# Kernel optimization log

Measured on AMD Instinct MI355X. Metric: run time of the kernel, lower is better.

Reference implementation:

```python
import jax, jax.numpy as jnp
import numpy as np

N = 20000      # nodes
E = 320000     # edges
IN = 128       # in_channels
HID = 64       # hidden_channels (per-head out dim, concat=False -> mean over heads)
HEADS = 4
NEG_SLOPE = 0.2


def setup_inputs() -> dict:
    key = jax.random.key(0)
    ks = jax.random.split(key, 18)
    g = lambda i, shape: jax.random.normal(ks[i], shape, dtype=jnp.float32) * 0.05
    return {
        "x": jax.random.normal(ks[0], (N, IN), dtype=jnp.float32),
        "edge_index": jax.random.randint(ks[1], (2, E), 0, N),
        # GATConv params: lin weight (no bias in PyG lin), att_src/att_dst, out bias
        "W0": g(2, (IN, HEADS * HID)),
        "W1": g(3, (HID, HEADS * HID)),
        "W2": g(4, (HID, HEADS * HID)),
        "W3": g(5, (HID, HEADS * HID)),
        "a_src": g(6, (4, HEADS, HID)),
        "a_dst": g(7, (4, HEADS, HID)),
        "gat_b": g(8, (4, HID)),
        # residual projection for layer 0 (in_channels != hidden_channels)
        "res_W": g(9, (IN, HID)),
        "res_b": g(10, (HID,)),
        # edge classifier MLP: 2*HID -> HID -> HID -> 1
        "lin_W0": g(11, (2 * HID, HID)),
        "lin_b0": g(12, (HID,)),
        "lin_W1": g(13, (HID, HID)),
        "lin_b1": g(14, (HID,)),
        "lin_W2": g(15, (HID, 1)),
        "lin_b2": g(16, (1,)),
    }


def gat_conv(x, src, dst, W, asrc, adst, b, n):
    # x: [n, F_in]; src/dst: [E_tot] (self-loops included); W: [F_in, H*C]
    h = (x @ W).reshape(n, HEADS, HID)                     # [n, H, C]
    s_src = (h * asrc).sum(-1)                             # [n, H]
    s_dst = (h * adst).sum(-1)                             # [n, H]
    e = jax.nn.leaky_relu(s_src[src] + s_dst[dst], NEG_SLOPE)  # [E_tot, H]
    # segment softmax over incoming edges of each dst node
    m = jax.ops.segment_max(e, dst, num_segments=n)        # [n, H]
    p = jnp.exp(e - m[dst])
    z = jax.ops.segment_sum(p, dst, num_segments=n)
    alpha = p / z[dst]                                     # [E_tot, H]
    out = jax.ops.segment_sum(alpha[:, :, None] * h[src], dst, num_segments=n)  # [n, H, C]
    return out.mean(axis=1) + b                            # concat=False -> mean over heads


def reference(x, edge_index, W0, W1, W2, W3, a_src, a_dst, gat_b,
              res_W, res_b, lin_W0, lin_b0, lin_W1, lin_b1, lin_W2, lin_b2):
    n = x.shape[0]
    loop = jnp.arange(n)
    src = jnp.concatenate([edge_index[0], loop])  # PyG GATConv adds self-loops
    dst = jnp.concatenate([edge_index[1], loop])
    Ws = [W0, W1, W2, W3]
    h = x
    for i in range(4):
        h_prev = h
        h = gat_conv(h, src, dst, Ws[i], a_src[i], a_dst[i], gat_b[i], n)
        if i == 0:
            h = h + h_prev @ res_W + res_b   # projected residual
        else:
            h = h + h_prev
        h = jax.nn.elu(h)
    row, col = edge_index[0], edge_index[1]
    er = jnp.concatenate([h[row], h[col]], axis=1)        # [E, 2*HID]
    er = jax.nn.relu(er @ lin_W0 + lin_b0)                # shapes differ -> no residual
    er = jax.nn.relu(er @ lin_W1 + lin_b1 + er)           # shapes match -> residual
    logits = er @ lin_W2 + lin_b2                          # [E, 1]
    return logits
```

## Files before the change

kernel.cpp:

```cpp
#include <hip/hip_runtime.h>
#include <hip/hip_bf16.h>

#define NSLOPE 0.2f
#define MAXDEG 64

typedef short bf16x8 __attribute__((ext_vector_type(8)));
typedef float f32x4 __attribute__((ext_vector_type(4)));

__device__ __forceinline__ unsigned short f2b(float f) {
    unsigned u = __float_as_uint(f);
    unsigned r = (u + 0x7FFFu + ((u >> 16) & 1u)) >> 16;
    return (unsigned short)r;
}
__device__ __forceinline__ float b2f_lo(unsigned w) {
    return __uint_as_float(w << 16);
}
__device__ __forceinline__ float b2f_hi(unsigned w) {
    return __uint_as_float(w & 0xFFFF0000u);
}
__device__ __forceinline__ float b2f_s(short s) {
    return __uint_as_float(((unsigned)(unsigned short)s) << 16);
}
__device__ __forceinline__ unsigned packb(float lo, float hi) {
    return ((unsigned)f2b(hi) << 16) | (unsigned)f2b(lo);
}

__global__ __launch_bounds__(256) void prep_all(
    const float* __restrict__ W0, const float* __restrict__ W1,
    const float* __restrict__ W2, const float* __restrict__ W3,
    const float* __restrict__ resW, const float* __restrict__ linW0,
    const float* __restrict__ linW1, const float* __restrict__ linB0,
    const float* __restrict__ a_src, const float* __restrict__ a_dst,
    const float* __restrict__ gat_b, const float* __restrict__ res_b,
    short* __restrict__ WtC0e, short* __restrict__ WtC1,
    short* __restrict__ WtC2, short* __restrict__ WtC3,
    short* __restrict__ WtUV, short* __restrict__ WbT,
    float* __restrict__ wsd0, float* __restrict__ wsdL,
    float* __restrict__ bias128, float* __restrict__ gb0res,
    int* __restrict__ deg, int n) {
    const int bx = blockIdx.x;
    const int tid = threadIdx.x;
    if (bx == 0) {
        for (int idx = blockIdx.y * 256 + tid; idx < 64 * 640; idx += 256 * 16) {
            int j = idx / 640, k = idx - j * 640;
            float v;
            if (k < 512) {
                int h = k >> 7, kk = k & 127;
                v = W0[kk * 256 + h * 64 + j];
            } else {
                v = resW[(k - 512) * 64 + j];
            }
            WtC0e[idx] = (short)f2b(v);
        }
    } else if (bx <= 3) {
        const float* src = (bx == 1) ? W1 : (bx == 2) ? W2 : W3;
        short* dst = (bx == 1) ? WtC1 : (bx == 2) ? WtC2 : WtC3;
        for (int idx = blockIdx.y * 256 + tid; idx < 64 * 256; idx += 256 * 16) {
            int j = idx >> 8, rem = idx & 255;
            int h = rem >> 6, kk = rem & 63;
            dst[idx] = (short)f2b(src[kk * 256 + h * 64 + j]);
        }
    } else if (bx == 4) {
        if (blockIdx.y) return;
        for (int idx = tid; idx < 64 * 64; idx += 256) {
            int nn = idx >> 6, k = idx & 63;
            WtUV[idx] = (short)f2b(linW0[k * 64 + nn]);
        }
    } else if (bx == 5) {
        if (blockIdx.y) return;
        for (int idx = tid; idx < 64 * 64; idx += 256) {
            int nn = idx >> 6, k = idx & 63;
            WtUV[64 * 64 + idx] = (short)f2b(linW0[(k + 64) * 64 + nn]);
        }
    } else if (bx == 6) {
        if (blockIdx.y) return;
        for (int idx = tid; idx < 64 * 64; idx += 256) {
            int nn = idx >> 6, k = idx & 63;
            WbT[idx] = (short)f2b(linW1[k * 64 + nn]);
        }
    } else if (bx == 7) {
        if (blockIdx.y) return;
        if (tid < 128)
            bias128[tid] = (tid < 64) ? linB0[tid] : 0.f;
        else if (tid < 192)
            gb0res[tid - 128] = gat_b[tid - 128] + res_b[tid - 128];
    } else if (bx <= 11) {
        if (blockIdx.y) return;
        int l = bx - 8;
        const float* W = (l == 0) ? W0 : (l == 1) ? W1 : (l == 2) ? W2 : W3;
        const int K = (l == 0) ? 128 : 64;
        float* dst = (l == 0) ? wsd0 : wsdL + (l - 1) * 64 * 8;
        for (int idx = tid; idx < K * 8; idx += 256) {
            int k = idx >> 3, j = idx & 7, h = j & 3;
            const float* av = ((j < 4) ? a_src : a_dst) + l * 256 + h * 64;
            const float* wr = W + k * 256 + h * 64;
            float s = 0.f;
#pragma unroll 8
            for (int c = 0; c < 64; ++c) s += wr[c] * av[c];
            dst[k * 8 + j] = s;
        }
    } else {
        for (int i = blockIdx.y * 256 + tid; i < n; i += 256 * 16) deg[i] = 0;
    }
}

__global__ __launch_bounds__(256) void fill_convert(
    const int* __restrict__ ei, int* __restrict__ deg, int* __restrict__ csrS,
    int E, const float* __restrict__ x, const float* __restrict__ wsd0,
    unsigned* __restrict__ xb2, float* __restrict__ Ssrc,
    float* __restrict__ Sdst, int n, int eBlocks) {
    if ((int)blockIdx.x < eBlocks) {
        int e = blockIdx.x * 256 + threadIdx.x;
        if (e >= E) return;
        int s = ei[e], d = ei[E + e];
        int pos = atomicAdd(&deg[d], 1);
        if (pos < MAXDEG) csrS[d * MAXDEG + pos] = s;
        return;
    }
    const int nb = blockIdx.x - eBlocks;
    const int wid = threadIdx.x >> 6;
    const int lane = threadIdx.x & 63;
    const int node = nb * 4 + wid;
    if (node >= n) return;
    float2 xv = *(const float2*)&x[(size_t)node * 128 + lane * 2];
    xb2[(size_t)node * 64 + lane] = packb(xv.x, xv.y);
    float pv[8];
    const float* w0 = &wsd0[(lane * 2) * 8];
    const float* w1 = &wsd0[(lane * 2 + 1) * 8];
#pragma unroll
    for (int j = 0; j < 8; ++j) pv[j] = xv.x * w0[j] + xv.y * w1[j];
#pragma unroll
    for (int off = 1; off < 64; off <<= 1) {
#pragma unroll
        for (int j = 0; j < 8; ++j) pv[j] += __shfl_xor(pv[j], off, 64);
    }
    if (lane == 0) {
        *(float4*)&Ssrc[node * 4] = make_float4(pv[0], pv[1], pv[2], pv[3]);
        *(float4*)&Sdst[node * 4] = make_float4(pv[4], pv[5], pv[6], pv[7]);
    }
}

__global__ __launch_bounds__(256) void gat_gather128(
    const int* __restrict__ csrS, const int* __restrict__ deg,
    const float* __restrict__ Ssrc, const float* __restrict__ Sdst,
    const unsigned* __restrict__ xin, unsigned* __restrict__ aggB, int n) {
    __shared__ __align__(16) float qs[4][64][4];
    __shared__ int sjs[4][64];
    const int wid = threadIdx.x >> 6;
    const int lane = threadIdx.x & 63;
    const int node = blockIdx.x * 4 + wid;
    if (node >= n) return;
    const int dn = min(deg[node], MAXDEG);
    const int sreg = (lane < dn) ? csrS[node * MAXDEG + lane] : 0;
    const float4 sd = *(const float4*)&Sdst[node * 4];
    const float4 ss = *(const float4*)&Ssrc[node * 4];
    float c0 = ss.x + sd.x, c1 = ss.y + sd.y, c2 = ss.z + sd.z,
          c3 = ss.w + sd.w;
    c0 = c0 > 0.f ? c0 : NSLOPE * c0;
    c1 = c1 > 0.f ? c1 : NSLOPE * c1;
    c2 = c2 > 0.f ? c2 : NSLOPE * c2;
    c3 = c3 > 0.f ? c3 : NSLOPE * c3;
    float ps0 = __expf(c0), ps1 = __expf(c1), ps2 = __expf(c2),
          ps3 = __expf(c3);
    float4 sv = *(const float4*)&Ssrc[sreg * 4];
    float e0 = sv.x + sd.x, e1 = sv.y + sd.y;
    float e2 = sv.z + sd.z, e3 = sv.w + sd.w;
    e0 = e0 > 0.f ? e0 : NSLOPE * e0;
    e1 = e1 > 0.f ? e1 : NSLOPE * e1;
    e2 = e2 > 0.f ? e2 : NSLOPE * e2;
    e3 = e3 > 0.f ? e3 : NSLOPE * e3;
    const bool act = lane < dn;
    float q0 = act ? __expf(e0) : 0.f;
    float q1 = act ? __expf(e1) : 0.f;
    float q2 = act ? __expf(e2) : 0.f;
    float q3 = act ? __expf(e3) : 0.f;
    *(float4*)&qs[wid][lane][0] = make_float4(q0, q1, q2, q3);
    sjs[wid][lane] = sreg;
    float z0 = q0, z1 = q1, z2 = q2, z3 = q3;
#pragma unroll
    for (int off = 1; off < 64; off <<= 1) {
        z0 += __shfl_xor(z0, off, 64);
        z1 += __shfl_xor(z1, off, 64);
        z2 += __shfl_xor(z2, off, 64);
        z3 += __shfl_xor(z3, off, 64);
    }
    z0 += ps0; z1 += ps1; z2 += ps2; z3 += ps3;
    unsigned own = xin[(size_t)node * 64 + lane];
    float f0o = b2f_lo(own), f1o = b2f_hi(own);
    float u00 = ps0 * f0o, u01 = ps0 * f1o;
    float u10 = ps1 * f0o, u11 = ps1 * f1o;
    float u20 = ps2 * f0o, u21 = ps2 * f1o;
    float u30 = ps3 * f0o, u31 = ps3 * f1o;
#pragma unroll 4
    for (int p = 0; p < dn; ++p) {
        float4 qv = *(const float4*)&qs[wid][p][0];
        int sj = sjs[wid][p];
        unsigned fv = xin[(size_t)sj * 64 + lane];
        float f0 = b2f_lo(fv), f1 = b2f_hi(fv);
        u00 += qv.x * f0; u01 += qv.x * f1;
        u10 += qv.y * f0; u11 += qv.y * f1;
        u20 += qv.z * f0; u21 += qv.z * f1;
        u30 += qv.w * f0; u31 += qv.w * f1;
    }
    float i0 = 0.25f / z0, i1 = 0.25f / z1, i2 = 0.25f / z2, i3 = 0.25f / z3;
    size_t base = (size_t)node * 320;
    aggB[base + lane] = packb(u00 * i0, u01 * i0);
    aggB[base + 64 + lane] = packb(u10 * i1, u11 * i1);
    aggB[base + 128 + lane] = packb(u20 * i2, u21 * i2);
    aggB[base + 192 + lane] = packb(u30 * i3, u31 * i3);
    aggB[base + 256 + lane] = own;
}

__global__ __launch_bounds__(256) void gat_gather64(
    const int* __restrict__ csrS, const int* __restrict__ deg,
    const float* __restrict__ Ssrc, const float* __restrict__ Sdst,
    const unsigned* __restrict__ fin, unsigned* __restrict__ aggB, int n) {
    __shared__ __align__(16) float qs[4][64][4];
    __shared__ int sjs[4][64];
    const int wid = threadIdx.x >> 6;
    const int lane = threadIdx.x & 63;
    const int half = lane >> 5;
    const int cl = lane & 31;
    const int node = blockIdx.x * 4 + wid;
    if (node >= n) return;
    const int dn = min(deg[node], MAXDEG);
    const int sreg = (lane < dn) ? csrS[node * MAXDEG + lane] : 0;
    const float4 sd = *(const float4*)&Sdst[node * 4];
    const float4 ss = *(const float4*)&Ssrc[node * 4];
    float c0 = ss.x + sd.x, c1 = ss.y + sd.y, c2 = ss.z + sd.z,
          c3 = ss.w + sd.w;
    c0 = c0 > 0.f ? c0 : NSLOPE * c0;
    c1 = c1 > 0.f ? c1 : NSLOPE * c1;
    c2 = c2 > 0.f ? c2 : NSLOPE * c2;
    c3 = c3 > 0.f ? c3 : NSLOPE * c3;
    float ps0 = __expf(c0), ps1 = __expf(c1), ps2 = __expf(c2),
          ps3 = __expf(c3);
    float4 sv = *(const float4*)&Ssrc[sreg * 4];
    float e0 = sv.x + sd.x, e1 = sv.y + sd.y;
    float e2 = sv.z + sd.z, e3 = sv.w + sd.w;
    e0 = e0 > 0.f ? e0 : NSLOPE * e0;
    e1 = e1 > 0.f ? e1 : NSLOPE * e1;
    e2 = e2 > 0.f ? e2 : NSLOPE * e2;
    e3 = e3 > 0.f ? e3 : NSLOPE * e3;
    const bool act = lane < dn;
    float q0 = act ? __expf(e0) : 0.f;
    float q1 = act ? __expf(e1) : 0.f;
    float q2 = act ? __expf(e2) : 0.f;
    float q3 = act ? __expf(e3) : 0.f;
    *(float4*)&qs[wid][lane][0] = make_float4(q0, q1, q2, q3);
    sjs[wid][lane] = sreg;
    float z0 = q0, z1 = q1, z2 = q2, z3 = q3;
#pragma unroll
    for (int off = 1; off < 64; off <<= 1) {
        z0 += __shfl_xor(z0, off, 64);
        z1 += __shfl_xor(z1, off, 64);
        z2 += __shfl_xor(z2, off, 64);
        z3 += __shfl_xor(z3, off, 64);
    }
    z0 += ps0; z1 += ps1; z2 += ps2; z3 += ps3;
    unsigned own = fin[(size_t)node * 32 + cl];
    float u00 = 0.f, u01 = 0.f, u10 = 0.f, u11 = 0.f;
    float u20 = 0.f, u21 = 0.f, u30 = 0.f, u31 = 0.f;
#pragma unroll 4
    for (int p = half; p < dn; p += 2) {
        float4 qv = *(const float4*)&qs[wid][p][0];
        int sj = sjs[wid][p];
        unsigned fv = fin[(size_t)sj * 32 + cl];
        float f0 = b2f_lo(fv), f1 = b2f_hi(fv);
        u00 += qv.x * f0; u01 += qv.x * f1;
        u10 += qv.y * f0; u11 += qv.y * f1;
        u20 += qv.z * f0; u21 += qv.z * f1;
        u30 += qv.w * f0; u31 += qv.w * f1;
    }
    u00 += __shfl_xor(u00, 32, 64); u01 += __shfl_xor(u01, 32, 64);
    u10 += __shfl_xor(u10, 32, 64); u11 += __shfl_xor(u11, 32, 64);
    u20 += __shfl_xor(u20, 32, 64); u21 += __shfl_xor(u21, 32, 64);
    u30 += __shfl_xor(u30, 32, 64); u31 += __shfl_xor(u31, 32, 64);
    float f0o = b2f_lo(own), f1o = b2f_hi(own);
    u00 += ps0 * f0o; u01 += ps0 * f1o;
    u10 += ps1 * f0o; u11 += ps1 * f1o;
    u20 += ps2 * f0o; u21 += ps2 * f1o;
    u30 += ps3 * f0o; u31 += ps3 * f1o;
    float i0 = 0.25f / z0, i1 = 0.25f / z1;
    float i2 = 0.25f / z2, i3 = 0.25f / z3;
    size_t base = (size_t)node * 128;
    if (half == 0) {
        aggB[base + cl] = packb(u00 * i0, u01 * i0);
        aggB[base + 32 + cl] = packb(u10 * i1, u11 * i1);
    } else {
        aggB[base + 64 + cl] = packb(u20 * i2, u21 * i2);
        aggB[base + 96 + cl] = packb(u30 * i3, u31 * i3);
    }
}

template <int KK, bool SCORES>
__global__ __launch_bounds__(256) void gemm_layer(
    const short* __restrict__ Xb, const short* __restrict__ Wt,
    const float* __restrict__ gbias, const float* __restrict__ resid,
    const float* __restrict__ wsd, float* __restrict__ feat,
    short* __restrict__ featb, float* __restrict__ Ssrc,
    float* __restrict__ Sdst, int n) {
    __shared__ __align__(16) short Xs[64 * 136];
    __shared__ __align__(16) short Ws[64 * 40];
    const int tid = threadIdx.x;
    const int nb = blockIdx.x * 64;
    const int wid = tid >> 6;
    const int lane = tid & 63;
    const int t = lane & 15, quad = lane >> 4;
    f32x4 acc[4];
#pragma unroll
    for (int g = 0; g < 4; ++g) acc[g] = (f32x4){0.f, 0.f, 0.f, 0.f};
#pragma unroll 1
    for (int c0 = 0; c0 < KK / 128; ++c0) {
        __syncthreads();
        for (int idx = tid; idx < 1024; idx += 256) {
            int row = idx >> 4, c = idx & 15;
            uint4 v = make_uint4(0, 0, 0, 0);
            if (nb + row < n)
                v = *(const uint4*)(Xb + (size_t)(nb + row) * KK + c0 * 128 +
                                    c * 8);
            *(uint4*)(Xs + row * 136 + c * 8) = v;
        }
#pragma unroll 1
        for (int kc = 0; kc < 4; ++kc) {
            __syncthreads();
            {
                int row = tid >> 2, c = tid & 3;
                uint4 v = *(const uint4*)(Wt + (size_t)row * KK + c0 * 128 +
                                          kc * 32 + c * 8);
                *(uint4*)(Ws + row * 40 + c * 8) = v;
            }
            __syncthreads();
            bf16x8 a =
                *(const bf16x8*)(Xs + (wid * 16 + t) * 136 + kc * 32 + quad * 8);
#pragma unroll
            for (int g = 0; g < 4; ++g) {
                bf16x8 b = *(const bf16x8*)(Ws + (g * 16 + t) * 40 + quad * 8);
                acc[g] =
                    __builtin_amdgcn_mfma_f32_16x16x32_bf16(a, b, acc[g], 0, 0, 0);
            }
        }
    }
    float bv[4];
#pragma unroll
    for (int g = 0; g < 4; ++g) bv[g] = gbias[g * 16 + t];
    float wsv[4][8];
    if (SCORES) {
#pragma unroll
        for (int g = 0; g < 4; ++g) {
            float4 lo = *(const float4*)&wsd[(g * 16 + t) * 8];
            float4 hi = *(const float4*)&wsd[(g * 16 + t) * 8 + 4];
            wsv[g][0] = lo.x; wsv[g][1] = lo.y; wsv[g][2] = lo.z;
            wsv[g][3] = lo.w; wsv[g][4] = hi.x; wsv[g][5] = hi.y;
            wsv[g][6] = hi.z; wsv[g][7] = hi.w;
        }
    }
#pragma unroll
    for (int r = 0; r < 4; ++r) {
        int node = nb + wid * 16 + quad * 4 + r;
        bool ok = node < n;
        float val[4];
#pragma unroll
        for (int g = 0; g < 4; ++g) {
            float v = acc[g][r] + bv[g];
            if (resid && ok) v += resid[(size_t)node * 64 + g * 16 + t];
            v = v > 0.f ? v : expm1f(v);
            val[g] = v;
            if (ok) {
                feat[(size_t)node * 64 + g * 16 + t] = v;
                featb[(size_t)node * 64 + g * 16 + t] = (short)f2b(v);
            }
        }
        if (SCORES) {
            float pv[8];
#pragma unroll
            for (int j = 0; j < 8; ++j) {
                pv[j] = val[0] * wsv[0][j] + val[1] * wsv[1][j] +
                        val[2] * wsv[2][j] + val[3] * wsv[3][j];
            }
#pragma unroll
            for (int off = 1; off < 16; off <<= 1) {
#pragma unroll
                for (int j = 0; j < 8; ++j) pv[j] += __shfl_xor(pv[j], off, 64);
            }
            if (t == 0 && ok) {
                *(float4*)&Ssrc[node * 4] =
                    make_float4(pv[0], pv[1], pv[2], pv[3]);
                *(float4*)&Sdst[node * 4] =
                    make_float4(pv[4], pv[5], pv[6], pv[7]);
            }
        }
    }
}

__global__ __launch_bounds__(256) void gemm_layer_uv(
    const short* __restrict__ Xb, const short* __restrict__ Wt,
    const float* __restrict__ gbias, const float* __restrict__ resid,
    const short* __restrict__ WtUV, const float* __restrict__ bias128,
    short* __restrict__ OutUV, int n) {
    constexpr int KK = 256;
    __shared__ __align__(16) short Xs[64 * 136];
    __shared__ __align__(16) short Ws[128 * 40];
    const int tid = threadIdx.x;
    const int nb = blockIdx.x * 64;
    const int wid = tid >> 6;
    const int lane = tid & 63;
    const int t = lane & 15, quad = lane >> 4;
    f32x4 acc[4];
#pragma unroll
    for (int g = 0; g < 4; ++g) acc[g] = (f32x4){0.f, 0.f, 0.f, 0.f};
#pragma unroll 1
    for (int c0 = 0; c0 < KK / 128; ++c0) {
        __syncthreads();
        for (int idx = tid; idx < 1024; idx += 256) {
            int row = idx >> 4, c = idx & 15;
            uint4 v = make_uint4(0, 0, 0, 0);
            if (nb + row < n)
                v = *(const uint4*)(Xb + (size_t)(nb + row) * KK + c0 * 128 +
                                    c * 8);
            *(uint4*)(Xs + row * 136 + c * 8) = v;
        }
#pragma unroll 1
        for (int kc = 0; kc < 4; ++kc) {
            __syncthreads();
            {
                int row = tid >> 2, c = tid & 3;
                uint4 v = *(const uint4*)(Wt + (size_t)row * KK + c0 * 128 +
                                          kc * 32 + c * 8);
                *(uint4*)(Ws + row * 40 + c * 8) = v;
            }
            __syncthreads();
            bf16x8 a =
                *(const bf16x8*)(Xs + (wid * 16 + t) * 136 + kc * 32 + quad * 8);
#pragma unroll
            for (int g = 0; g < 4; ++g) {
                bf16x8 b = *(const bf16x8*)(Ws + (g * 16 + t) * 40 + quad * 8);
                acc[g] =
                    __builtin_amdgcn_mfma_f32_16x16x32_bf16(a, b, acc[g], 0, 0, 0);
            }
        }
    }
    float bv[4];
#pragma unroll
    for (int g = 0; g < 4; ++g) bv[g] = gbias[g * 16 + t];
    __syncthreads();
#pragma unroll
    for (int r = 0; r < 4; ++r) {
        int node = nb + wid * 16 + quad * 4 + r;
        bool ok = node < n;
        int lrow = wid * 16 + quad * 4 + r;
#pragma unroll
        for (int g = 0; g < 4; ++g) {
            float v = acc[g][r] + bv[g];
            if (ok) v += resid[(size_t)node * 64 + g * 16 + t];
            v = v > 0.f ? v : expm1f(v);
            Xs[lrow * 72 + g * 16 + t] = (short)f2b(v);
        }
    }
    f32x4 acc2[8];
#pragma unroll
    for (int g = 0; g < 8; ++g) acc2[g] = (f32x4){0.f, 0.f, 0.f, 0.f};
#pragma unroll 1
    for (int kc = 0; kc < 2; ++kc) {
        __syncthreads();
        for (int idx = tid; idx < 512; idx += 256) {
            int row = idx >> 2, c = idx & 3;
            uint4 v = *(const uint4*)(WtUV + (size_t)row * 64 + kc * 32 + c * 8);
            *(uint4*)(Ws + row * 40 + c * 8) = v;
        }
        __syncthreads();
        bf16x8 a = *(const bf16x8*)(Xs + (wid * 16 + t) * 72 + kc * 32 + quad * 8);
#pragma unroll
        for (int g = 0; g < 8; ++g) {
            bf16x8 b = *(const bf16x8*)(Ws + (g * 16 + t) * 40 + quad * 8);
            acc2[g] = __builtin_amdgcn_mfma_f32_16x16x32_bf16(a, b, acc2[g], 0, 0, 0);
        }
    }
    float b2[8];
#pragma unroll
    for (int g = 0; g < 8; ++g) b2[g] = bias128[g * 16 + t];
#pragma unroll
    for (int r = 0; r < 4; ++r) {
        int node = nb + wid * 16 + quad * 4 + r;
        if (node >= n) continue;
#pragma unroll
        for (int g = 0; g < 8; ++g)
            OutUV[(size_t)node * 128 + g * 16 + t] =
                (short)f2b(acc2[g][r] + b2[g]);
    }
}

__global__ __launch_bounds__(256) void edge_mlp3(
    const int* __restrict__ ei, const unsigned* __restrict__ UV,
    const short* __restrict__ WbT, const float* __restrict__ bb,
    const float* __restrict__ Wc, const float* __restrict__ bc,
    float* __restrict__ out, int E) {
    __shared__ __align__(16) short t1b[64 * 72];
    __shared__ __align__(16) short wbs[64 * 72];
    const int tid = threadIdx.x;
    const int eBase = blockIdx.x * 64;
    for (int idx = tid; idx < 512; idx += 256) {
        int row = idx >> 3, c = idx & 7;
        *(uint4*)(wbs + row * 72 + c * 8) =
            *(const uint4*)(WbT + row * 64 + c * 8);
    }
    {
        const int j = tid & 31;
        const int eg = tid >> 5;
        int rr[8], cc[8];
#pragma unroll
        for (int it = 0; it < 8; ++it) {
            int e = eBase + it * 8 + eg;
            rr[it] = (e < E) ? ei[e] : 0;
            cc[it] = (e < E) ? ei[E + e] : 0;
        }
#pragma unroll
        for (int it = 0; it < 8; ++it) {
            unsigned uu = UV[(size_t)rr[it] * 64 + j];
            unsigned vv = UV[(size_t)cc[it] * 64 + 32 + j];
            float lo = fmaxf(b2f_lo(uu) + b2f_lo(vv), 0.f);
            float hi = fmaxf(b2f_hi(uu) + b2f_hi(vv), 0.f);
            *(unsigned*)(t1b + (it * 8 + eg) * 72 + j * 2) = packb(lo, hi);
        }
    }
    __syncthreads();
    const int w = tid >> 6, lane = tid & 63;
    const int t = lane & 15, quad = lane >> 4;
    f32x4 acc[4];
#pragma unroll
    for (int g = 0; g < 4; ++g) acc[g] = (f32x4){0.f, 0.f, 0.f, 0.f};
#pragma unroll
    for (int kc = 0; kc < 2; ++kc) {
        bf16x8 a = *(const bf16x8*)(t1b + (w * 16 + t) * 72 + kc * 32 + quad * 8);
#pragma unroll
        for (int g = 0; g < 4; ++g) {
            bf16x8 b = *(const bf16x8*)(wbs + (g * 16 + t) * 72 + kc * 32 + quad * 8);
            acc[g] = __builtin_amdgcn_mfma_f32_16x16x32_bf16(a, b, acc[g], 0, 0, 0);
        }
    }
    float wcv[4], bbv[4];
#pragma unroll
    for (int g = 0; g < 4; ++g) {
        wcv[g] = Wc[g * 16 + t];
        bbv[g] = bb[g * 16 + t];
    }
    const float bcv = bc[0];
#pragma unroll
    for (int r = 0; r < 4; ++r) {
        int el = w * 16 + quad * 4 + r;
        float part = 0.f;
#pragma unroll
        for (int g = 0; g < 4; ++g) {
            float t1v = b2f_s(t1b[el * 72 + g * 16 + t]);
            float t2 = fmaxf(acc[g][r] + bbv[g] + t1v, 0.f);
            part += t2 * wcv[g];
        }
        part += __shfl_xor(part, 1, 64);
        part += __shfl_xor(part, 2, 64);
        part += __shfl_xor(part, 4, 64);
        part += __shfl_xor(part, 8, 64);
        int e = eBase + el;
        if (t == 0 && e < E) out[e] = part + bcv;
    }
}

extern "C" void kernel_launch(void* const* d_in, const int* in_sizes, int n_in,
                              void* d_out, int out_size, void* d_ws,
                              size_t ws_size, hipStream_t stream) {
    const float* x = (const float*)d_in[0];
    const int* ei = (const int*)d_in[1];
    const float* W0 = (const float*)d_in[2];
    const float* W1 = (const float*)d_in[3];
    const float* W2 = (const float*)d_in[4];
    const float* W3 = (const float*)d_in[5];
    const float* a_src = (const float*)d_in[6];
    const float* a_dst = (const float*)d_in[7];
    const float* gat_b = (const float*)d_in[8];
    const float* res_W = (const float*)d_in[9];
    const float* res_b = (const float*)d_in[10];
    const float* lin_W0 = (const float*)d_in[11];
    const float* lin_b0 = (const float*)d_in[12];
    const float* lin_W1 = (const float*)d_in[13];
    const float* lin_b1 = (const float*)d_in[14];
    const float* lin_W2 = (const float*)d_in[15];
    const float* lin_b2 = (const float*)d_in[16];
    float* out = (float*)d_out;

    const int N = in_sizes[0] / 128;
    const int E = in_sizes[1] / 2;

    char* ws = (char*)d_ws;
    unsigned* aggB = (unsigned*)ws;
    float* featA = (float*)(aggB + (size_t)N * 320);
    float* featB = featA + (size_t)N * 64;
    unsigned* xb2 = (unsigned*)(featB + (size_t)N * 64);
    unsigned* featbA = xb2 + (size_t)N * 64;
    unsigned* featbB = featbA + (size_t)N * 32;
    unsigned* UVb = featbB + (size_t)N * 32;
    float* Ssrc = (float*)(UVb + (size_t)N * 64);
    float* Sdst = Ssrc + (size_t)N * 4;
    short* WtC0e = (short*)(Sdst + (size_t)N * 4);
    short* WtC1 = WtC0e + 64 * 640;
    short* WtC2 = WtC1 + 64 * 256;
    short* WtC3 = WtC2 + 64 * 256;
    short* WtUV = WtC3 + 64 * 256;
    short* WbT = WtUV + 128 * 64;
    float* wsd0 = (float*)(WbT + 64 * 64);
    float* wsdL = wsd0 + 128 * 8;
    float* bias128 = wsdL + 3 * 64 * 8;
    float* gb0res = bias128 + 128;
    int* deg = (int*)(gb0res + 64);
    int* csrS = deg + N;

    const int gemmBlocks = (N + 63) / 64;
    const int eBlocks = (E + 255) / 256;
    const int nodeW = (N + 3) / 4;

    prep_all<<<dim3(13, 16), 256, 0, stream>>>(
        W0, W1, W2, W3, res_W, lin_W0, lin_W1, lin_b0, a_src, a_dst, gat_b,
        res_b, WtC0e, WtC1, WtC2, WtC3, WtUV, WbT, wsd0, wsdL, bias128,
        gb0res, deg, N);
    fill_convert<<<eBlocks + nodeW, 256, 0, stream>>>(
        ei, deg, csrS, E, x, wsd0, xb2, Ssrc, Sdst, N, eBlocks);

    gat_gather128<<<nodeW, 256, 0, stream>>>(csrS, deg, Ssrc, Sdst, xb2, aggB,
                                             N);
    gemm_layer<640, true><<<gemmBlocks, 256, 0, stream>>>(
        (const short*)aggB, WtC0e, gb0res, nullptr, wsdL, featA,
        (short*)featbA, Ssrc, Sdst, N);

    gat_gather64<<<nodeW, 256, 0, stream>>>(csrS, deg, Ssrc, Sdst, featbA,
                                            aggB, N);
    gemm_layer<256, true><<<gemmBlocks, 256, 0, stream>>>(
        (const short*)aggB, WtC1, gat_b + 64, featA, wsdL + 64 * 8, featB,
        (short*)featbB, Ssrc, Sdst, N);
    gat_gather64<<<nodeW, 256, 0, stream>>>(csrS, deg, Ssrc, Sdst, featbB,
                                            aggB, N);
    gemm_layer<256, true><<<gemmBlocks, 256, 0, stream>>>(
        (const short*)aggB, WtC2, gat_b + 128, featB, wsdL + 2 * 64 * 8,
        featA, (short*)featbA, Ssrc, Sdst, N);

    gat_gather64<<<nodeW, 256, 0, stream>>>(csrS, deg, Ssrc, Sdst, featbA,
                                            aggB, N);
    gemm_layer_uv<<<gemmBlocks, 256, 0, stream>>>(
        (const short*)aggB, WtC3, gat_b + 192, featA, WtUV, bias128,
        (short*)UVb, N);

    edge_mlp3<<<(E + 63) / 64, 256, 0, stream>>>(ei, UVb, WbT, lin_b1, lin_W2,
                                                 lin_b2, out, E);
}
```

Before: 293.6 us.

## Shrink GEMM tiles to 32 rows and stage full 128-wide weight chunk per sync

The node GEMM kernels now use 128-thread blocks covering 32 rows, which doubles the block count for better occupancy on a small N. Each block loads the whole 128-wide K chunk of the weight into shared memory at once, so the four per-kc syncthreads pairs collapse into one. The UV projection weights are likewise loaded in a single pass. The cost is more shared memory per block and more redundant weight loads across the larger number of blocks.

```diff
diff --git a/kernel.cpp b/kernel.cpp
--- a/kernel.cpp
+++ b/kernel.cpp
@@ -294,16 +294,16 @@
 }
 
 template <int KK, bool SCORES>
-__global__ __launch_bounds__(256) void gemm_layer(
+__global__ __launch_bounds__(128) void gemm_layer(
     const short* __restrict__ Xb, const short* __restrict__ Wt,
     const float* __restrict__ gbias, const float* __restrict__ resid,
     const float* __restrict__ wsd, float* __restrict__ feat,
     short* __restrict__ featb, float* __restrict__ Ssrc,
     float* __restrict__ Sdst, int n) {
-    __shared__ __align__(16) short Xs[64 * 136];
-    __shared__ __align__(16) short Ws[64 * 40];
+    __shared__ __align__(16) short Xs[32 * 136];
+    __shared__ __align__(16) short Ws[64 * 136];
     const int tid = threadIdx.x;
-    const int nb = blockIdx.x * 64;
+    const int nb = blockIdx.x * 32;
     const int wid = tid >> 6;
     const int lane = tid & 63;
     const int t = lane & 15, quad = lane >> 4;
@@ -313,7 +313,7 @@
 #pragma unroll 1
     for (int c0 = 0; c0 < KK / 128; ++c0) {
         __syncthreads();
-        for (int idx = tid; idx < 1024; idx += 256) {
+        for (int idx = tid; idx < 512; idx += 128) {
             int row = idx >> 4, c = idx & 15;
             uint4 v = make_uint4(0, 0, 0, 0);
             if (nb + row < n)
@@ -321,21 +321,20 @@
                                     c * 8);
             *(uint4*)(Xs + row * 136 + c * 8) = v;
         }
-#pragma unroll 1
+        for (int idx = tid; idx < 1024; idx += 128) {
+            int row = idx >> 4, c = idx & 15;
+            *(uint4*)(Ws + row * 136 + c * 8) =
+                *(const uint4*)(Wt + (size_t)row * KK + c0 * 128 + c * 8);
+        }
+        __syncthreads();
+#pragma unroll
         for (int kc = 0; kc < 4; ++kc) {
-            __syncthreads();
-            {
-                int row = tid >> 2, c = tid & 3;
-                uint4 v = *(const uint4*)(Wt + (size_t)row * KK + c0 * 128 +
-                                          kc * 32 + c * 8);
-                *(uint4*)(Ws + row * 40 + c * 8) = v;
-            }
-            __syncthreads();
             bf16x8 a =
                 *(const bf16x8*)(Xs + (wid * 16 + t) * 136 + kc * 32 + quad * 8);
 #pragma unroll
             for (int g = 0; g < 4; ++g) {
-                bf16x8 b = *(const bf16x8*)(Ws + (g * 16 + t) * 40 + quad * 8);
+                bf16x8 b = *(const bf16x8*)(Ws + (g * 16 + t) * 136 + kc * 32 +
+                                            quad * 8);
                 acc[g] =
                     __builtin_amdgcn_mfma_f32_16x16x32_bf16(a, b, acc[g], 0, 0, 0);
             }
@@ -393,16 +392,16 @@
     }
 }
 
-__global__ __launch_bounds__(256) void gemm_layer_uv(
+__global__ __launch_bounds__(128) void gemm_layer_uv(
     const short* __restrict__ Xb, const short* __restrict__ Wt,
     const float* __restrict__ gbias, const float* __restrict__ resid,
     const short* __restrict__ WtUV, const float* __restrict__ bias128,
     short* __restrict__ OutUV, int n) {
     constexpr int KK = 256;
-    __shared__ __align__(16) short Xs[64 * 136];
-    __shared__ __align__(16) short Ws[128 * 40];
+    __shared__ __align__(16) short Xs[32 * 136];
+    __shared__ __align__(16) short Ws[128 * 72];
     const int tid = threadIdx.x;
-    const int nb = blockIdx.x * 64;
+    const int nb = blockIdx.x * 32;
     const int wid = tid >> 6;
     const int lane = tid & 63;
     const int t = lane & 15, quad = lane >> 4;
@@ -412,7 +411,7 @@
 #pragma unroll 1
     for (int c0 = 0; c0 < KK / 128; ++c0) {
         __syncthreads();
-        for (int idx = tid; idx < 1024; idx += 256) {
+        for (int idx = tid; idx < 512; idx += 128) {
             int row = idx >> 4, c = idx & 15;
             uint4 v = make_uint4(0, 0, 0, 0);
             if (nb + row < n)
@@ -420,21 +419,20 @@
                                     c * 8);
             *(uint4*)(Xs + row * 136 + c * 8) = v;
         }
-#pragma unroll 1
+        for (int idx = tid; idx < 1024; idx += 128) {
+            int row = idx >> 4, c = idx & 15;
+            *(uint4*)(Ws + row * 136 + c * 8) =
+                *(const uint4*)(Wt + (size_t)row * KK + c0 * 128 + c * 8);
+        }
+        __syncthreads();
+#pragma unroll
         for (int kc = 0; kc < 4; ++kc) {
-            __syncthreads();
-            {
-                int row = tid >> 2, c = tid & 3;
-                uint4 v = *(const uint4*)(Wt + (size_t)row * KK + c0 * 128 +
-                                          kc * 32 + c * 8);
-                *(uint4*)(Ws + row * 40 + c * 8) = v;
-            }
-            __syncthreads();
             bf16x8 a =
                 *(const bf16x8*)(Xs + (wid * 16 + t) * 136 + kc * 32 + quad * 8);
 #pragma unroll
             for (int g = 0; g < 4; ++g) {
-                bf16x8 b = *(const bf16x8*)(Ws + (g * 16 + t) * 40 + quad * 8);
+                bf16x8 b = *(const bf16x8*)(Ws + (g * 16 + t) * 136 + kc * 32 +
+                                            quad * 8);
                 acc[g] =
                     __builtin_amdgcn_mfma_f32_16x16x32_bf16(a, b, acc[g], 0, 0, 0);
             }
@@ -444,6 +442,11 @@
 #pragma unroll
     for (int g = 0; g < 4; ++g) bv[g] = gbias[g * 16 + t];
     __syncthreads();
+    for (int idx = tid; idx < 1024; idx += 128) {
+        int row = idx >> 3, c = idx & 7;
+        *(uint4*)(Ws + row * 72 + c * 8) =
+            *(const uint4*)(WtUV + (size_t)row * 64 + c * 8);
+    }
 #pragma unroll
     for (int r = 0; r < 4; ++r) {
         int node = nb + wid * 16 + quad * 4 + r;
@@ -454,25 +457,21 @@
             float v = acc[g][r] + bv[g];
             if (ok) v += resid[(size_t)node * 64 + g * 16 + t];
             v = v > 0.f ? v : expm1f(v);
-            Xs[lrow * 72 + g * 16 + t] = (short)f2b(v);
-        }
-    }
+            Xs[lrow * 136 + g * 16 + t] = (short)f2b(v);
+        }
+    }
+    __syncthreads();
     f32x4 acc2[8];
 #pragma unroll
     for (int g = 0; g < 8; ++g) acc2[g] = (f32x4){0.f, 0.f, 0.f, 0.f};
-#pragma unroll 1
+#pragma unroll
     for (int kc = 0; kc < 2; ++kc) {
-        __syncthreads();
-        for (int idx = tid; idx < 512; idx += 256) {
-            int row = idx >> 2, c = idx & 3;
-            uint4 v = *(const uint4*)(WtUV + (size_t)row * 64 + kc * 32 + c * 8);
-            *(uint4*)(Ws + row * 40 + c * 8) = v;
-        }
-        __syncthreads();
-        bf16x8 a = *(const bf16x8*)(Xs + (wid * 16 + t) * 72 + kc * 32 + quad * 8);
+        bf16x8 a =
+            *(const bf16x8*)(Xs + (wid * 16 + t) * 136 + kc * 32 + quad * 8);
 #pragma unroll
         for (int g = 0; g < 8; ++g) {
-            bf16x8 b = *(const bf16x8*)(Ws + (g * 16 + t) * 40 + quad * 8);
+            bf16x8 b =
+                *(const bf16x8*)(Ws + (g * 16 + t) * 72 + kc * 32 + quad * 8);
             acc2[g] = __builtin_amdgcn_mfma_f32_16x16x32_bf16(a, b, acc2[g], 0, 0, 0);
         }
     }
@@ -612,7 +611,7 @@
     int* deg = (int*)(gb0res + 64);
     int* csrS = deg + N;
 
-    const int gemmBlocks = (N + 63) / 64;
+    const int gemmBlocks = (N + 31) / 32;
     const int eBlocks = (E + 255) / 256;
     const int nodeW = (N + 3) / 4;
 
@@ -625,24 +624,24 @@
 
     gat_gather128<<<nodeW, 256, 0, stream>>>(csrS, deg, Ssrc, Sdst, xb2, aggB,
                                              N);
-    gemm_layer<640, true><<<gemmBlocks, 256, 0, stream>>>(
+    gemm_layer<640, true><<<gemmBlocks, 128, 0, stream>>>(
         (const short*)aggB, WtC0e, gb0res, nullptr, wsdL, featA,
         (short*)featbA, Ssrc, Sdst, N);
 
     gat_gather64<<<nodeW, 256, 0, stream>>>(csrS, deg, Ssrc, Sdst, featbA,
                                             aggB, N);
-    gemm_layer<256, true><<<gemmBlocks, 256, 0, stream>>>(
+    gemm_layer<256, true><<<gemmBlocks, 128, 0, stream>>>(
         (const short*)aggB, WtC1, gat_b + 64, featA, wsdL + 64 * 8, featB,
         (short*)featbB, Ssrc, Sdst, N);
     gat_gather64<<<nodeW, 256, 0, stream>>>(csrS, deg, Ssrc, Sdst, featbB,
                                             aggB, N);
-    gemm_layer<256, true><<<gemmBlocks, 256, 0, stream>>>(
+    gemm_layer<256, true><<<gemmBlocks, 128, 0, stream>>>(
         (const short*)aggB, WtC2, gat_b + 128, featB, wsdL + 2 * 64 * 8,
         featA, (short*)featbA, Ssrc, Sdst, N);
 
     gat_gather64<<<nodeW, 256, 0, stream>>>(csrS, deg, Ssrc, Sdst, featbA,
                                             aggB, N);
-    gemm_layer_uv<<<gemmBlocks, 256, 0, stream>>>(
+    gemm_layer_uv<<<gemmBlocks, 128, 0, stream>>>(
         (const short*)aggB, WtC3, gat_b + 192, featA, WtUV, bias128,
         (short*)UVb, N);
 
```

Result: slower. 306.2 us (+4.3%).
